# Performance work log

Hardware: AMD Instinct MI355X
Metric: run time of the kernel (lower is better)

## Reference

```python
import jax, jax.numpy as jnp
import numpy as np

N_NODES = 100000
N_EDGES = 1600000
N_GRAPHS = 2048
IN_DIM = 128
HIDDEN = 128
OUT_DIM = 3


def setup_inputs() -> dict:
    key = jax.random.key(0)
    ks = jax.random.split(key, 16)
    x = jax.random.normal(ks[0], (N_NODES, IN_DIM), dtype=jnp.float32)
    edge_index = jax.random.randint(ks[1], (2, N_EDGES), 0, N_NODES, dtype=jnp.int64)
    batch = jnp.sort(jax.random.randint(ks[2], (N_NODES,), 0, N_GRAPHS, dtype=jnp.int64))
    s = 0.02
    return {
        "x": x,
        "edge_index": edge_index,
        "batch": batch,
        # GINConv MLP: Linear(in,hidden) -> ReLU -> Linear(hidden,hidden)
        "gin_w1": jax.random.normal(ks[3], (IN_DIM, HIDDEN), dtype=jnp.float32) * s,
        "gin_b1": jnp.zeros((HIDDEN,), dtype=jnp.float32),
        "gin_w2": jax.random.normal(ks[4], (HIDDEN, HIDDEN), dtype=jnp.float32) * s,
        "gin_b2": jnp.zeros((HIDDEN,), dtype=jnp.float32),
        # GCNConv weight + bias
        "gcn_w": jax.random.normal(ks[5], (HIDDEN, HIDDEN), dtype=jnp.float32) * s,
        "gcn_b": jnp.zeros((HIDDEN,), dtype=jnp.float32),
        # head
        "lin1_w": jax.random.normal(ks[6], (HIDDEN, HIDDEN), dtype=jnp.float32) * s,
        "lin1_b": jnp.zeros((HIDDEN,), dtype=jnp.float32),
        "lin2_w": jax.random.normal(ks[7], (HIDDEN, OUT_DIM), dtype=jnp.float32) * s,
        "lin2_b": jnp.zeros((OUT_DIM,), dtype=jnp.float32),
    }


def reference(x, edge_index, batch, gin_w1, gin_b1, gin_w2, gin_b2,
              gcn_w, gcn_b, lin1_w, lin1_b, lin2_w, lin2_b):
    src, dst = edge_index[0], edge_index[1]

    # ---- GINConv (eps=0): h_i = MLP(x_i + sum_{j in N(i)} x_j) ----
    agg = jax.ops.segment_sum(x[src], dst, num_segments=N_NODES)  # [N, in_dim]
    h = agg + x  # (1 + eps) * x with eps = 0
    h = jax.nn.relu(h @ gin_w1 + gin_b1) @ gin_w2 + gin_b2
    h = jax.nn.relu(h)  # outer F.relu

    # ---- GCNConv with self-loops and symmetric normalization ----
    # deg_i = (# incoming edges to i) + 1 (self-loop)
    ones_e = jnp.ones((N_EDGES,), dtype=h.dtype)
    deg = jax.ops.segment_sum(ones_e, dst, num_segments=N_NODES) + 1.0
    dinv = jax.lax.rsqrt(deg)  # deg >= 1 always
    hw = h @ gcn_w  # [N, hidden]
    norm_e = dinv[src] * dinv[dst]  # [E]
    msg = jax.ops.segment_sum(norm_e[:, None] * hw[src], dst, num_segments=N_NODES)
    h = msg + (dinv * dinv)[:, None] * hw + gcn_b  # self-loop contribution
    h = jax.nn.relu(h)

    # ---- global_add_pool over graphs ----
    g = jax.ops.segment_sum(h, batch, num_segments=N_GRAPHS)  # [G, hidden]

    g = jax.nn.relu(g @ lin1_w + lin1_b)
    return g @ lin2_w + lin2_b  # [G, out_dim]
```

## Files before the change

kernel.cpp:

```cpp
#include <hip/hip_runtime.h>
#include <hip/hip_bf16.h>

#define N_NODES  100000
#define N_EDGES  1600000
#define N_GRAPHS 2048
#define DIM      128
#define ELLW     64

__device__ __forceinline__ unsigned short f2b(float f) {
    unsigned u = __float_as_uint(f);
    u += 0x7FFFu + ((u >> 16) & 1u);
    return (unsigned short)(u >> 16);
}
__device__ __forceinline__ float b2f(unsigned short h) {
    return __uint_as_float(((unsigned)h) << 16);
}
__device__ __forceinline__ float4 dec4(ushort4 h) {
    return make_float4(b2f(h.x), b2f(h.y), b2f(h.z), b2f(h.w));
}

typedef __attribute__((ext_vector_type(8))) short bfrag;
typedef __attribute__((ext_vector_type(4))) float ffrag;

__global__ __launch_bounds__(256)
void cast_bf16(const float* __restrict__ in, unsigned short* __restrict__ out,
               int* __restrict__ cursor,
               const float* __restrict__ Wa, unsigned short* __restrict__ Ta,
               const float* __restrict__ Wb, unsigned short* __restrict__ Tb,
               const float* __restrict__ Wc, unsigned short* __restrict__ Tc,
               int n8)
{
    int i = blockIdx.x * 256 + threadIdx.x;
    if (i < N_NODES) cursor[i] = 0;
    if (i < 3 * DIM * DIM) {
        int which = i >> 14;
        int idx   = i & (DIM * DIM - 1);
        const float* W = (which == 0) ? Wa : (which == 1) ? Wb : Wc;
        unsigned short* T = (which == 0) ? Ta : (which == 1) ? Tb : Tc;
        int k = idx >> 7, n = idx & 127;
        T[n * DIM + k] = f2b(W[idx]);
    }
    if (i >= n8) return;
    const float4* in4 = (const float4*)in;
    float4 a = in4[i * 2 + 0];
    float4 b = in4[i * 2 + 1];
    uint4 q;
    q.x = (unsigned)f2b(a.x) | ((unsigned)f2b(a.y) << 16);
    q.y = (unsigned)f2b(a.z) | ((unsigned)f2b(a.w) << 16);
    q.z = (unsigned)f2b(b.x) | ((unsigned)f2b(b.y) << 16);
    q.w = (unsigned)f2b(b.z) | ((unsigned)f2b(b.w) << 16);
    ((uint4*)out)[i] = q;
}

#define FILL_RANGES 8
#define FILL_RSIZE  (N_NODES / FILL_RANGES)

__global__ __launch_bounds__(256)
void ell_fill(const int* __restrict__ src, const int* __restrict__ dst,
              int* __restrict__ cursor, int* __restrict__ ell,
              float* __restrict__ g, int E)
{
    int gid = blockIdx.x * 256 + threadIdx.x;
    g[gid] = 0.f;

    const int r = blockIdx.x & (FILL_RANGES - 1);
    const int s = blockIdx.x >> 3;
    const int nslice = gridDim.x >> 3;
    const unsigned lo = (unsigned)(r * FILL_RSIZE);
    const int stride = nslice * 256 * 4;

    for (int e0 = (s * 256 + threadIdx.x) * 4; e0 < E; e0 += stride) {
        int4 d  = *(const int4*)&dst[e0];
        int4 sv = *(const int4*)&src[e0];
        if ((unsigned)(d.x - lo) < (unsigned)FILL_RSIZE) {
            int p = atomicAdd(&cursor[d.x], 1); ell[d.x * ELLW + p] = sv.x;
        }
        if ((unsigned)(d.y - lo) < (unsigned)FILL_RSIZE) {
            int p = atomicAdd(&cursor[d.y], 1); ell[d.y * ELLW + p] = sv.y;
        }
        if ((unsigned)(d.z - lo) < (unsigned)FILL_RSIZE) {
            int p = atomicAdd(&cursor[d.z], 1); ell[d.z * ELLW + p] = sv.z;
        }
        if ((unsigned)(d.w - lo) < (unsigned)FILL_RSIZE) {
            int p = atomicAdd(&cursor[d.w], 1); ell[d.w * ELLW + p] = sv.w;
        }
    }
}

__global__ __launch_bounds__(256)
void ell_gather_bb(const int* __restrict__ deg, const int* __restrict__ ell,
                   const unsigned short* __restrict__ Vb,
                   unsigned short* __restrict__ Out,
                   float* __restrict__ dinv, int N)
{
    int node = blockIdx.x * 8 + (threadIdx.x >> 5);
    int lane = threadIdx.x & 31;
    if (node >= N) return;
    int dn = deg[node];
    if (lane == 0) dinv[node] = rsqrtf((float)dn + 1.0f);
    const int* row = ell + node * ELLW;
    const ushort4* V4 = (const ushort4*)Vb;
    float4 acc = dec4(V4[(size_t)node * 32 + lane]);
    int e = 0;
    for (; e + 8 <= dn; e += 8) {
        int s0 = row[e + 0], s1 = row[e + 1], s2 = row[e + 2], s3 = row[e + 3];
        int s4 = row[e + 4], s5 = row[e + 5], s6 = row[e + 6], s7 = row[e + 7];
        float4 v0 = dec4(V4[(size_t)s0 * 32 + lane]);
        float4 v1 = dec4(V4[(size_t)s1 * 32 + lane]);
        float4 v2 = dec4(V4[(size_t)s2 * 32 + lane]);
        float4 v3 = dec4(V4[(size_t)s3 * 32 + lane]);
        float4 v4 = dec4(V4[(size_t)s4 * 32 + lane]);
        float4 v5 = dec4(V4[(size_t)s5 * 32 + lane]);
        float4 v6 = dec4(V4[(size_t)s6 * 32 + lane]);
        float4 v7 = dec4(V4[(size_t)s7 * 32 + lane]);
        acc.x += (v0.x + v1.x + v2.x + v3.x) + (v4.x + v5.x + v6.x + v7.x);
        acc.y += (v0.y + v1.y + v2.y + v3.y) + (v4.y + v5.y + v6.y + v7.y);
        acc.z += (v0.z + v1.z + v2.z + v3.z) + (v4.z + v5.z + v6.z + v7.z);
        acc.w += (v0.w + v1.w + v2.w + v3.w) + (v4.w + v5.w + v6.w + v7.w);
    }
    for (; e + 4 <= dn; e += 4) {
        int s0 = row[e + 0], s1 = row[e + 1], s2 = row[e + 2], s3 = row[e + 3];
        float4 v0 = dec4(V4[(size_t)s0 * 32 + lane]);
        float4 v1 = dec4(V4[(size_t)s1 * 32 + lane]);
        float4 v2 = dec4(V4[(size_t)s2 * 32 + lane]);
        float4 v3 = dec4(V4[(size_t)s3 * 32 + lane]);
        acc.x += v0.x + v1.x + v2.x + v3.x;
        acc.y += v0.y + v1.y + v2.y + v3.y;
        acc.z += v0.z + v1.z + v2.z + v3.z;
        acc.w += v0.w + v1.w + v2.w + v3.w;
    }
    for (; e < dn; ++e) {
        int s = row[e];
        float4 v = dec4(V4[(size_t)s * 32 + lane]);
        acc.x += v.x; acc.y += v.y; acc.z += v.z; acc.w += v.w;
    }
    ushort4 o;
    o.x = f2b(acc.x); o.y = f2b(acc.y); o.z = f2b(acc.z); o.w = f2b(acc.w);
    ((ushort4*)Out)[(size_t)node * 32 + lane] = o;
}

#define MLP_ROWS 64
#define HBST     136

__global__ __launch_bounds__(256)
void mlp3_mfma(const unsigned short* __restrict__ Hg,
               const unsigned short* __restrict__ w1t, const float* __restrict__ b1,
               const unsigned short* __restrict__ w2t, const float* __restrict__ b2,
               const unsigned short* __restrict__ w3t, const float* __restrict__ dinv,
               unsigned short* __restrict__ ub_out, int N)
{
    __shared__ unsigned short Hb[MLP_ROWS][HBST];
    __shared__ unsigned short Ws[DIM][HBST];

    const int tid  = threadIdx.x;
    const int wave = tid >> 6;
    const int lane = tid & 63;
    const int row0 = blockIdx.x * MLP_ROWS;

#pragma unroll
    for (int l = 0; l < 4; ++l) {
        int f  = tid + l * 256;
        int r  = f >> 4;
        int c8 = (f & 15) << 3;
        int gr = row0 + r;
        uint4 v = make_uint4(0u, 0u, 0u, 0u);
        if (gr < N) v = *(const uint4*)&Hg[(size_t)gr * DIM + c8];
        *(uint4*)&Hb[r][c8] = v;
    }

    const int m0 = wave * 16;
    const int qa = lane >> 4;
    const int la = lane & 15;

    for (int layer = 0; layer < 3; ++layer) {
        const unsigned short* __restrict__ Wt =
            (layer == 0) ? w1t : (layer == 1) ? w2t : w3t;

        __syncthreads();
#pragma unroll
        for (int l = 0; l < 8; ++l) {
            int f  = tid + l * 256;
            int r  = f >> 4;
            int c8 = (f & 15) << 3;
            *(uint4*)&Ws[r][c8] = *(const uint4*)&Wt[(size_t)r * DIM + c8];
        }
        __syncthreads();

        bfrag afr[4];
#pragma unroll
        for (int kc = 0; kc < 4; ++kc)
            afr[kc] = *(const bfrag*)&Hb[m0 + la][kc * 32 + qa * 8];

        if (layer < 2) {
            const float* bias = (layer == 0) ? b1 : b2;
#pragma unroll
            for (int nt = 0; nt < 8; ++nt) {
                const int n0 = nt * 16;
                ffrag acc = {0.f, 0.f, 0.f, 0.f};
#pragma unroll
                for (int kc = 0; kc < 4; ++kc) {
                    bfrag bfr = *(const bfrag*)&Ws[n0 + la][kc * 32 + qa * 8];
                    acc = __builtin_amdgcn_mfma_f32_16x16x32_bf16(afr[kc], bfr, acc, 0, 0, 0);
                }
                float bn = bias[n0 + la];
#pragma unroll
                for (int r = 0; r < 4; ++r) {
                    float v = fmaxf(acc[r] + bn, 0.f);
                    Hb[m0 + qa * 4 + r][n0 + la] = f2b(v);
                }
            }
        } else {
            float dv[4];
#pragma unroll
            for (int r = 0; r < 4; ++r) {
                int gr = row0 + m0 + qa * 4 + r;
                dv[r] = (gr < N) ? dinv[gr] : 0.f;
            }
#pragma unroll
            for (int nt = 0; nt < 8; ++nt) {
                const int n0 = nt * 16;
                ffrag acc = {0.f, 0.f, 0.f, 0.f};
#pragma unroll
                for (int kc = 0; kc < 4; ++kc) {
                    bfrag bfr = *(const bfrag*)&Ws[n0 + la][kc * 32 + qa * 8];
                    acc = __builtin_amdgcn_mfma_f32_16x16x32_bf16(afr[kc], bfr, acc, 0, 0, 0);
                }
#pragma unroll
                for (int r = 0; r < 4; ++r) {
                    int gr = row0 + m0 + qa * 4 + r;
                    if (gr < N)
                        ub_out[(size_t)gr * DIM + n0 + la] = f2b(dv[r] * acc[r]);
                }
            }
        }
    }
}

#define P2_NODES 64
__global__ __launch_bounds__(256)
void gcn_gather_pool(const int* __restrict__ deg, const int* __restrict__ ell,
                     const unsigned short* __restrict__ ub,
                     const float* __restrict__ bias, const int* __restrict__ batch,
                     float* __restrict__ g, int N)
{
    const int grp  = threadIdx.x >> 5;
    const int lane = threadIdx.x & 31;
    const int n0   = blockIdx.x * P2_NODES + grp * 8;
    const ushort4* V4 = (const ushort4*)ub;

    float4 bj;
    bj.x = bias[lane * 4 + 0];
    bj.y = bias[lane * 4 + 1];
    bj.z = bias[lane * 4 + 2];
    bj.w = bias[lane * 4 + 3];

    float4 lsum = make_float4(0.f, 0.f, 0.f, 0.f);
    int prev = -1;

    for (int k = 0; k < 8; ++k) {
        int node = n0 + k;
        if (node >= N) break;
        int dn = deg[node];
        const int* row = ell + node * ELLW;
        float4 acc = dec4(V4[(size_t)node * 32 + lane]);
        int e = 0;
        for (; e + 8 <= dn; e += 8) {
            int s0 = row[e + 0], s1 = row[e + 1], s2 = row[e + 2], s3 = row[e + 3];
            int s4 = row[e + 4], s5 = row[e + 5], s6 = row[e + 6], s7 = row[e + 7];
            float4 v0 = dec4(V4[(size_t)s0 * 32 + lane]);
            float4 v1 = dec4(V4[(size_t)s1 * 32 + lane]);
            float4 v2 = dec4(V4[(size_t)s2 * 32 + lane]);
            float4 v3 = dec4(V4[(size_t)s3 * 32 + lane]);
            float4 v4 = dec4(V4[(size_t)s4 * 32 + lane]);
            float4 v5 = dec4(V4[(size_t)s5 * 32 + lane]);
            float4 v6 = dec4(V4[(size_t)s6 * 32 + lane]);
            float4 v7 = dec4(V4[(size_t)s7 * 32 + lane]);
            acc.x += (v0.x + v1.x + v2.x + v3.x) + (v4.x + v5.x + v6.x + v7.x);
            acc.y += (v0.y + v1.y + v2.y + v3.y) + (v4.y + v5.y + v6.y + v7.y);
            acc.z += (v0.z + v1.z + v2.z + v3.z) + (v4.z + v5.z + v6.z + v7.z);
            acc.w += (v0.w + v1.w + v2.w + v3.w) + (v4.w + v5.w + v6.w + v7.w);
        }
        for (; e + 4 <= dn; e += 4) {
            int s0 = row[e + 0], s1 = row[e + 1], s2 = row[e + 2], s3 = row[e + 3];
            float4 v0 = dec4(V4[(size_t)s0 * 32 + lane]);
            float4 v1 = dec4(V4[(size_t)s1 * 32 + lane]);
            float4 v2 = dec4(V4[(size_t)s2 * 32 + lane]);
            float4 v3 = dec4(V4[(size_t)s3 * 32 + lane]);
            acc.x += v0.x + v1.x + v2.x + v3.x;
            acc.y += v0.y + v1.y + v2.y + v3.y;
            acc.z += v0.z + v1.z + v2.z + v3.z;
            acc.w += v0.w + v1.w + v2.w + v3.w;
        }
        for (; e < dn; ++e) {
            int s = row[e];
            float4 v = dec4(V4[(size_t)s * 32 + lane]);
            acc.x += v.x; acc.y += v.y; acc.z += v.z; acc.w += v.w;
        }
        float di = rsqrtf((float)dn + 1.0f);
        float4 h;
        h.x = fmaxf(fmaf(di, acc.x, bj.x), 0.f);
        h.y = fmaxf(fmaf(di, acc.y, bj.y), 0.f);
        h.z = fmaxf(fmaf(di, acc.z, bj.z), 0.f);
        h.w = fmaxf(fmaf(di, acc.w, bj.w), 0.f);

        int b = batch[node];
        if (b != prev) {
            if (prev >= 0) {
                float* gp = &g[(size_t)prev * DIM + lane * 4];
                atomicAdd(gp + 0, lsum.x);
                atomicAdd(gp + 1, lsum.y);
                atomicAdd(gp + 2, lsum.z);
                atomicAdd(gp + 3, lsum.w);
            }
            lsum = make_float4(0.f, 0.f, 0.f, 0.f);
            prev = b;
        }
        lsum.x += h.x; lsum.y += h.y; lsum.z += h.z; lsum.w += h.w;
    }
    if (prev >= 0) {
        float* gp = &g[(size_t)prev * DIM + lane * 4];
        atomicAdd(gp + 0, lsum.x);
        atomicAdd(gp + 1, lsum.y);
        atomicAdd(gp + 2, lsum.z);
        atomicAdd(gp + 3, lsum.w);
    }
}

__global__ __launch_bounds__(128)
void head_kernel(const float* __restrict__ g, const float* __restrict__ w1,
                 const float* __restrict__ b1, const float* __restrict__ w2,
                 const float* __restrict__ b2, float* __restrict__ out)
{
    __shared__ float gs[DIM];
    __shared__ float red[6];
    int gid = blockIdx.x;
    int t = threadIdx.x;

    gs[t] = g[(size_t)gid * DIM + t];
    __syncthreads();

    float acc = b1[t];
#pragma unroll
    for (int k = 0; k < DIM; ++k) acc = fmaf(gs[k], w1[k * DIM + t], acc);
    float h = fmaxf(acc, 0.f);

    float c0 = h * w2[t * 3 + 0];
    float c1 = h * w2[t * 3 + 1];
    float c2 = h * w2[t * 3 + 2];
#pragma unroll
    for (int off = 32; off >= 1; off >>= 1) {
        c0 += __shfl_down(c0, off);
        c1 += __shfl_down(c1, off);
        c2 += __shfl_down(c2, off);
    }
    int wave = t >> 6;
    if ((t & 63) == 0) {
        red[wave * 3 + 0] = c0;
        red[wave * 3 + 1] = c1;
        red[wave * 3 + 2] = c2;
    }
    __syncthreads();
    if (t == 0) {
        out[(size_t)gid * 3 + 0] = red[0] + red[3] + b2[0];
        out[(size_t)gid * 3 + 1] = red[1] + red[4] + b2[1];
        out[(size_t)gid * 3 + 2] = red[2] + red[5] + b2[2];
    }
}

extern "C" void kernel_launch(void* const* d_in, const int* in_sizes, int n_in,
                              void* d_out, int out_size, void* d_ws, size_t ws_size,
                              hipStream_t stream)
{
    const float* x       = (const float*)d_in[0];
    const int*   eidx    = (const int*)d_in[1];
    const int*   batch   = (const int*)d_in[2];
    const float* gin_w1  = (const float*)d_in[3];
    const float* gin_b1  = (const float*)d_in[4];
    const float* gin_w2  = (const float*)d_in[5];
    const float* gin_b2  = (const float*)d_in[6];
    const float* gcn_w   = (const float*)d_in[7];
    const float* gcn_b   = (const float*)d_in[8];
    const float* lin1_w  = (const float*)d_in[9];
    const float* lin1_b  = (const float*)d_in[10];
    const float* lin2_w  = (const float*)d_in[11];
    const float* lin2_b  = (const float*)d_in[12];

    const int* src = eidx;
    const int* dst = eidx + N_EDGES;

    const size_t NBH = (size_t)N_NODES * DIM * sizeof(unsigned short);
    const size_t WTB = (size_t)DIM * DIM * sizeof(unsigned short);
    char* base = (char*)d_ws;
    size_t off = 0;
    auto carve = [&](size_t bytes) {
        char* p = base + off;
        off = (off + bytes + 255) & ~(size_t)255;
        return p;
    };
    unsigned short* xb  = (unsigned short*)carve(NBH);
    unsigned short* hb  = (unsigned short*)carve(NBH);
    unsigned short* ub  = (unsigned short*)carve(NBH);
    unsigned short* w1t = (unsigned short*)carve(WTB);
    unsigned short* w2t = (unsigned short*)carve(WTB);
    unsigned short* w3t = (unsigned short*)carve(WTB);
    int*   cursor = (int*)  carve(N_NODES * sizeof(int));
    int*   ell    = (int*)  carve((size_t)N_NODES * ELLW * sizeof(int));
    float* dinv   = (float*)carve(N_NODES * sizeof(float));
    float* g      = (float*)carve((size_t)N_GRAPHS * DIM * sizeof(float));

    const int ngrid = (N_NODES + 7) / 8;
    const int mgrid = (N_NODES + MLP_ROWS - 1) / MLP_ROWS;
    const int pgrid = (N_NODES + P2_NODES - 1) / P2_NODES;

    cast_bf16<<<(N_NODES * DIM / 8 + 255) / 256, 256, 0, stream>>>(
        x, xb, cursor, gin_w1, w1t, gin_w2, w2t, gcn_w, w3t,
        N_NODES * DIM / 8);

    ell_fill<<<FILL_RANGES * 128, 256, 0, stream>>>(src, dst, cursor, ell,
                                                    g, N_EDGES);

    ell_gather_bb<<<ngrid, 256, 0, stream>>>(cursor, ell, xb, hb, dinv, N_NODES);

    mlp3_mfma<<<mgrid, 256, 0, stream>>>(hb, w1t, gin_b1, w2t, gin_b2,
                                         w3t, dinv, ub, N_NODES);

    gcn_gather_pool<<<pgrid, 256, 0, stream>>>(cursor, ell, ub, gcn_b,
                                               batch, g, N_NODES);

    head_kernel<<<N_GRAPHS, 128, 0, stream>>>(
        g, lin1_w, lin1_b, lin2_w, lin2_b, (float*)d_out);
}
```

Before: 363.4 us.

## Store GCN messages in scaled FP8 and fuse cast with ELL fill

The pre-normalized GCN features are now stored as FP8 e4m3 with a power-of-two scale instead of bf16. This halves the bytes fetched per neighbor in the bandwidth-bound gather-pool kernel, and the scale is undone when dinv is applied. Separately, the bf16 cast and the ELL fill kernels become one launch with disjoint block ranges, and the cursor reset moves to a memset. This risks accuracy loss from FP8 quantization and adds a memset launch.

```diff
diff --git a/kernel.cpp b/kernel.cpp
--- a/kernel.cpp
+++ b/kernel.cpp
@@ -1,5 +1,6 @@
 #include <hip/hip_runtime.h>
 #include <hip/hip_bf16.h>
+#include <hip/hip_fp8.h>
 
 #define N_NODES  100000
 #define N_EDGES  1600000
@@ -19,71 +20,99 @@
     return make_float4(b2f(h.x), b2f(h.y), b2f(h.z), b2f(h.w));
 }
 
+#define UB_SCALE     64.0f
+#define UB_INVSCALE  0.015625f
+
+__device__ __forceinline__ unsigned char f_to_fp8(float x) {
+#if __has_builtin(__builtin_amdgcn_cvt_pk_fp8_f32)
+    return (unsigned char)(__builtin_amdgcn_cvt_pk_fp8_f32(x, x, 0, false) & 0xff);
+#else
+    __hip_fp8_e4m3 q(x);
+    return q.__x;
+#endif
+}
+__device__ __forceinline__ float4 fp8x4_to_f4(unsigned p) {
+#if __has_builtin(__builtin_amdgcn_cvt_f32_fp8)
+    return make_float4(__builtin_amdgcn_cvt_f32_fp8((int)p, 0),
+                       __builtin_amdgcn_cvt_f32_fp8((int)p, 1),
+                       __builtin_amdgcn_cvt_f32_fp8((int)p, 2),
+                       __builtin_amdgcn_cvt_f32_fp8((int)p, 3));
+#else
+    __hip_fp8_e4m3 a, b, c, d;
+    a.__x = (unsigned char)(p & 0xff);
+    b.__x = (unsigned char)((p >> 8) & 0xff);
+    c.__x = (unsigned char)((p >> 16) & 0xff);
+    d.__x = (unsigned char)((p >> 24) & 0xff);
+    return make_float4((float)a, (float)b, (float)c, (float)d);
+#endif
+}
+
 typedef __attribute__((ext_vector_type(8))) short bfrag;
 typedef __attribute__((ext_vector_type(4))) float ffrag;
 
+#define FILL_RANGES 8
+#define FILL_RSIZE  (N_NODES / FILL_RANGES)
+#define CF_FILL_BLOCKS 1024
+#define CF_CAST_BLOCKS 6250
+
 __global__ __launch_bounds__(256)
-void cast_bf16(const float* __restrict__ in, unsigned short* __restrict__ out,
-               int* __restrict__ cursor,
+void cast_fill(const float* __restrict__ in, unsigned short* __restrict__ out,
                const float* __restrict__ Wa, unsigned short* __restrict__ Ta,
                const float* __restrict__ Wb, unsigned short* __restrict__ Tb,
                const float* __restrict__ Wc, unsigned short* __restrict__ Tc,
-               int n8)
-{
-    int i = blockIdx.x * 256 + threadIdx.x;
-    if (i < N_NODES) cursor[i] = 0;
-    if (i < 3 * DIM * DIM) {
-        int which = i >> 14;
-        int idx   = i & (DIM * DIM - 1);
-        const float* W = (which == 0) ? Wa : (which == 1) ? Wb : Wc;
-        unsigned short* T = (which == 0) ? Ta : (which == 1) ? Tb : Tc;
-        int k = idx >> 7, n = idx & 127;
-        T[n * DIM + k] = f2b(W[idx]);
-    }
-    if (i >= n8) return;
-    const float4* in4 = (const float4*)in;
-    float4 a = in4[i * 2 + 0];
-    float4 b = in4[i * 2 + 1];
-    uint4 q;
-    q.x = (unsigned)f2b(a.x) | ((unsigned)f2b(a.y) << 16);
-    q.y = (unsigned)f2b(a.z) | ((unsigned)f2b(a.w) << 16);
-    q.z = (unsigned)f2b(b.x) | ((unsigned)f2b(b.y) << 16);
-    q.w = (unsigned)f2b(b.z) | ((unsigned)f2b(b.w) << 16);
-    ((uint4*)out)[i] = q;
-}
-
-#define FILL_RANGES 8
-#define FILL_RSIZE  (N_NODES / FILL_RANGES)
-
-__global__ __launch_bounds__(256)
-void ell_fill(const int* __restrict__ src, const int* __restrict__ dst,
-              int* __restrict__ cursor, int* __restrict__ ell,
-              float* __restrict__ g, int E)
-{
-    int gid = blockIdx.x * 256 + threadIdx.x;
-    g[gid] = 0.f;
-
-    const int r = blockIdx.x & (FILL_RANGES - 1);
-    const int s = blockIdx.x >> 3;
-    const int nslice = gridDim.x >> 3;
-    const unsigned lo = (unsigned)(r * FILL_RSIZE);
-    const int stride = nslice * 256 * 4;
-
-    for (int e0 = (s * 256 + threadIdx.x) * 4; e0 < E; e0 += stride) {
-        int4 d  = *(const int4*)&dst[e0];
-        int4 sv = *(const int4*)&src[e0];
-        if ((unsigned)(d.x - lo) < (unsigned)FILL_RSIZE) {
-            int p = atomicAdd(&cursor[d.x], 1); ell[d.x * ELLW + p] = sv.x;
-        }
-        if ((unsigned)(d.y - lo) < (unsigned)FILL_RSIZE) {
-            int p = atomicAdd(&cursor[d.y], 1); ell[d.y * ELLW + p] = sv.y;
-        }
-        if ((unsigned)(d.z - lo) < (unsigned)FILL_RSIZE) {
-            int p = atomicAdd(&cursor[d.z], 1); ell[d.z * ELLW + p] = sv.z;
-        }
-        if ((unsigned)(d.w - lo) < (unsigned)FILL_RSIZE) {
-            int p = atomicAdd(&cursor[d.w], 1); ell[d.w * ELLW + p] = sv.w;
-        }
+               const int* __restrict__ src, const int* __restrict__ dst,
+               int* __restrict__ cursor, int* __restrict__ ell,
+               float* __restrict__ g, int E, int n8)
+{
+    const int bid = blockIdx.x;
+    const int t   = threadIdx.x;
+
+    if (bid < CF_FILL_BLOCKS) {
+        int gid = bid * 256 + t;
+        g[gid] = 0.f;
+
+        const int r = bid & (FILL_RANGES - 1);
+        const int s = bid >> 3;
+        const int nslice = CF_FILL_BLOCKS >> 3;
+        const unsigned lo = (unsigned)(r * FILL_RSIZE);
+        const int stride = nslice * 256 * 4;
+
+        for (int e0 = (s * 256 + t) * 4; e0 < E; e0 += stride) {
+            int4 d  = *(const int4*)&dst[e0];
+            int4 sv = *(const int4*)&src[e0];
+            if ((unsigned)(d.x - lo) < (unsigned)FILL_RSIZE) {
+                int p = atomicAdd(&cursor[d.x], 1); ell[d.x * ELLW + p] = sv.x;
+            }
+            if ((unsigned)(d.y - lo) < (unsigned)FILL_RSIZE) {
+                int p = atomicAdd(&cursor[d.y], 1); ell[d.y * ELLW + p] = sv.y;
+            }
+            if ((unsigned)(d.z - lo) < (unsigned)FILL_RSIZE) {
+                int p = atomicAdd(&cursor[d.z], 1); ell[d.z * ELLW + p] = sv.z;
+            }
+            if ((unsigned)(d.w - lo) < (unsigned)FILL_RSIZE) {
+                int p = atomicAdd(&cursor[d.w], 1); ell[d.w * ELLW + p] = sv.w;
+            }
+        }
+    } else {
+        int i = (bid - CF_FILL_BLOCKS) * 256 + t;
+        if (i < 3 * DIM * DIM) {
+            int which = i >> 14;
+            int idx   = i & (DIM * DIM - 1);
+            const float* W = (which == 0) ? Wa : (which == 1) ? Wb : Wc;
+            unsigned short* T = (which == 0) ? Ta : (which == 1) ? Tb : Tc;
+            int k = idx >> 7, n = idx & 127;
+            T[n * DIM + k] = f2b(W[idx]);
+        }
+        if (i >= n8) return;
+        const float4* in4 = (const float4*)in;
+        float4 a = in4[i * 2 + 0];
+        float4 b = in4[i * 2 + 1];
+        uint4 q;
+        q.x = (unsigned)f2b(a.x) | ((unsigned)f2b(a.y) << 16);
+        q.y = (unsigned)f2b(a.z) | ((unsigned)f2b(a.w) << 16);
+        q.z = (unsigned)f2b(b.x) | ((unsigned)f2b(b.y) << 16);
+        q.w = (unsigned)f2b(b.z) | ((unsigned)f2b(b.w) << 16);
+        ((uint4*)out)[i] = q;
     }
 }
 
@@ -147,7 +176,7 @@
                const unsigned short* __restrict__ w1t, const float* __restrict__ b1,
                const unsigned short* __restrict__ w2t, const float* __restrict__ b2,
                const unsigned short* __restrict__ w3t, const float* __restrict__ dinv,
-               unsigned short* __restrict__ ub_out, int N)
+               unsigned char* __restrict__ ub_out, int N)
 {
     __shared__ unsigned short Hb[MLP_ROWS][HBST];
     __shared__ unsigned short Ws[DIM][HBST];
@@ -214,7 +243,7 @@
 #pragma unroll
             for (int r = 0; r < 4; ++r) {
                 int gr = row0 + m0 + qa * 4 + r;
-                dv[r] = (gr < N) ? dinv[gr] : 0.f;
+                dv[r] = (gr < N) ? dinv[gr] * UB_SCALE : 0.f;
             }
 #pragma unroll
             for (int nt = 0; nt < 8; ++nt) {
@@ -229,7 +258,7 @@
                 for (int r = 0; r < 4; ++r) {
                     int gr = row0 + m0 + qa * 4 + r;
                     if (gr < N)
-                        ub_out[(size_t)gr * DIM + n0 + la] = f2b(dv[r] * acc[r]);
+                        ub_out[(size_t)gr * DIM + n0 + la] = f_to_fp8(dv[r] * acc[r]);
                 }
             }
         }
@@ -239,14 +268,14 @@
 #define P2_NODES 64
 __global__ __launch_bounds__(256)
 void gcn_gather_pool(const int* __restrict__ deg, const int* __restrict__ ell,
-                     const unsigned short* __restrict__ ub,
+                     const unsigned char* __restrict__ ub,
                      const float* __restrict__ bias, const int* __restrict__ batch,
                      float* __restrict__ g, int N)
 {
     const int grp  = threadIdx.x >> 5;
     const int lane = threadIdx.x & 31;
     const int n0   = blockIdx.x * P2_NODES + grp * 8;
-    const ushort4* V4 = (const ushort4*)ub;
+    const unsigned* U4 = (const unsigned*)ub;
 
     float4 bj;
     bj.x = bias[lane * 4 + 0];
@@ -262,19 +291,27 @@
         if (node >= N) break;
         int dn = deg[node];
         const int* row = ell + node * ELLW;
-        float4 acc = dec4(V4[(size_t)node * 32 + lane]);
+        float4 acc = fp8x4_to_f4(U4[(size_t)node * 32 + lane]);
         int e = 0;
         for (; e + 8 <= dn; e += 8) {
             int s0 = row[e + 0], s1 = row[e + 1], s2 = row[e + 2], s3 = row[e + 3];
             int s4 = row[e + 4], s5 = row[e + 5], s6 = row[e + 6], s7 = row[e + 7];
-            float4 v0 = dec4(V4[(size_t)s0 * 32 + lane]);
-            float4 v1 = dec4(V4[(size_t)s1 * 32 + lane]);
-            float4 v2 = dec4(V4[(size_t)s2 * 32 + lane]);
-            float4 v3 = dec4(V4[(size_t)s3 * 32 + lane]);
-            float4 v4 = dec4(V4[(size_t)s4 * 32 + lane]);
-            float4 v5 = dec4(V4[(size_t)s5 * 32 + lane]);
-            float4 v6 = dec4(V4[(size_t)s6 * 32 + lane]);
-            float4 v7 = dec4(V4[(size_t)s7 * 32 + lane]);
+            unsigned w0 = U4[(size_t)s0 * 32 + lane];
+            unsigned w1 = U4[(size_t)s1 * 32 + lane];
+            unsigned w2 = U4[(size_t)s2 * 32 + lane];
+            unsigned w3 = U4[(size_t)s3 * 32 + lane];
+            unsigned w4 = U4[(size_t)s4 * 32 + lane];
+            unsigned w5 = U4[(size_t)s5 * 32 + lane];
+            unsigned w6 = U4[(size_t)s6 * 32 + lane];
+            unsigned w7 = U4[(size_t)s7 * 32 + lane];
+            float4 v0 = fp8x4_to_f4(w0);
+            float4 v1 = fp8x4_to_f4(w1);
+            float4 v2 = fp8x4_to_f4(w2);
+            float4 v3 = fp8x4_to_f4(w3);
+            float4 v4 = fp8x4_to_f4(w4);
+            float4 v5 = fp8x4_to_f4(w5);
+            float4 v6 = fp8x4_to_f4(w6);
+            float4 v7 = fp8x4_to_f4(w7);
             acc.x += (v0.x + v1.x + v2.x + v3.x) + (v4.x + v5.x + v6.x + v7.x);
             acc.y += (v0.y + v1.y + v2.y + v3.y) + (v4.y + v5.y + v6.y + v7.y);
             acc.z += (v0.z + v1.z + v2.z + v3.z) + (v4.z + v5.z + v6.z + v7.z);
@@ -282,10 +319,10 @@
         }
         for (; e + 4 <= dn; e += 4) {
             int s0 = row[e + 0], s1 = row[e + 1], s2 = row[e + 2], s3 = row[e + 3];
-            float4 v0 = dec4(V4[(size_t)s0 * 32 + lane]);
-            float4 v1 = dec4(V4[(size_t)s1 * 32 + lane]);
-            float4 v2 = dec4(V4[(size_t)s2 * 32 + lane]);
-            float4 v3 = dec4(V4[(size_t)s3 * 32 + lane]);
+            float4 v0 = fp8x4_to_f4(U4[(size_t)s0 * 32 + lane]);
+            float4 v1 = fp8x4_to_f4(U4[(size_t)s1 * 32 + lane]);
+            float4 v2 = fp8x4_to_f4(U4[(size_t)s2 * 32 + lane]);
+            float4 v3 = fp8x4_to_f4(U4[(size_t)s3 * 32 + lane]);
             acc.x += v0.x + v1.x + v2.x + v3.x;
             acc.y += v0.y + v1.y + v2.y + v3.y;
             acc.z += v0.z + v1.z + v2.z + v3.z;
@@ -293,10 +330,10 @@
         }
         for (; e < dn; ++e) {
             int s = row[e];
-            float4 v = dec4(V4[(size_t)s * 32 + lane]);
+            float4 v = fp8x4_to_f4(U4[(size_t)s * 32 + lane]);
             acc.x += v.x; acc.y += v.y; acc.z += v.z; acc.w += v.w;
         }
-        float di = rsqrtf((float)dn + 1.0f);
+        float di = rsqrtf((float)dn + 1.0f) * UB_INVSCALE;
         float4 h;
         h.x = fmaxf(fmaf(di, acc.x, bj.x), 0.f);
         h.y = fmaxf(fmaf(di, acc.y, bj.y), 0.f);
@@ -389,6 +426,7 @@
     const int* dst = eidx + N_EDGES;
 
     const size_t NBH = (size_t)N_NODES * DIM * sizeof(unsigned short);
+    const size_t NB8 = (size_t)N_NODES * DIM;
     const size_t WTB = (size_t)DIM * DIM * sizeof(unsigned short);
     char* base = (char*)d_ws;
     size_t off = 0;
@@ -399,7 +437,7 @@
     };
     unsigned short* xb  = (unsigned short*)carve(NBH);
     unsigned short* hb  = (unsigned short*)carve(NBH);
-    unsigned short* ub  = (unsigned short*)carve(NBH);
+    unsigned char*  ub8 = (unsigned char*) carve(NB8);
     unsigned short* w1t = (unsigned short*)carve(WTB);
     unsigned short* w2t = (unsigned short*)carve(WTB);
     unsigned short* w3t = (unsigned short*)carve(WTB);
@@ -412,19 +450,17 @@
     const int mgrid = (N_NODES + MLP_ROWS - 1) / MLP_ROWS;
     const int pgrid = (N_NODES + P2_NODES - 1) / P2_NODES;
 
-    cast_bf16<<<(N_NODES * DIM / 8 + 255) / 256, 256, 0, stream>>>(
-        x, xb, cursor, gin_w1, w1t, gin_w2, w2t, gcn_w, w3t,
-        N_NODES * DIM / 8);
-
-    ell_fill<<<FILL_RANGES * 128, 256, 0, stream>>>(src, dst, cursor, ell,
-                                                    g, N_EDGES);
+    hipMemsetAsync(cursor, 0, N_NODES * sizeof(int), stream);
+    cast_fill<<<CF_FILL_BLOCKS + CF_CAST_BLOCKS, 256, 0, stream>>>(
+        x, xb, gin_w1, w1t, gin_w2, w2t, gcn_w, w3t,
+        src, dst, cursor, ell, g, N_EDGES, N_NODES * DIM / 8);
 
     ell_gather_bb<<<ngrid, 256, 0, stream>>>(cursor, ell, xb, hb, dinv, N_NODES);
 
     mlp3_mfma<<<mgrid, 256, 0, stream>>>(hb, w1t, gin_b1, w2t, gin_b2,
-                                         w3t, dinv, ub, N_NODES);
-
-    gcn_gather_pool<<<pgrid, 256, 0, stream>>>(cursor, ell, ub, gcn_b,
+                                         w3t, dinv, ub8, N_NODES);
+
+    gcn_gather_pool<<<pgrid, 256, 0, stream>>>(cursor, ell, ub8, gcn_b,
                                                batch, g, N_NODES);
 
     head_kernel<<<N_GRAPHS, 128, 0, stream>>>(
```

Measured after the change: 332.6 us. -8.5%, faster.
